# Optimization experiments

Measured on AMD Instinct MI355X. Metric: run time of the kernel, lower is better.

The kernel has to match this reference:

```python
import jax, jax.numpy as jnp
import numpy as np

S = 3      # num_subset
CI = 64    # inter_channels
C = 256    # in_channels == out_channels
T = 400    # num_frame
V = 25     # num_node


def make_pe(channel, joint_num, time_len, domain):
    if domain == 'temporal':
        pos = np.repeat(np.arange(time_len), joint_num).astype(np.float32)
    else:
        pos = np.tile(np.arange(joint_num), time_len).astype(np.float32)
    pe = np.zeros((time_len * joint_num, channel), dtype=np.float32)
    div = np.exp(np.arange(0, channel, 2, dtype=np.float32) * (-np.log(10000.0) / channel))
    pe[:, 0::2] = np.sin(pos[:, None] * div[None, :])
    pe[:, 1::2] = np.cos(pos[:, None] * div[None, :])
    pe = pe.reshape(time_len, joint_num, channel).transpose(2, 0, 1)[None]  # (1,C,T,V)
    return jnp.asarray(pe)


def setup_inputs() -> dict:
    key = jax.random.key(0)
    ks = jax.random.split(key, 10)
    def w(k, shape):
        return jax.random.normal(k, shape, jnp.float32) * 0.02
    return {
        'x': jax.random.normal(ks[0], (4, C, T, V), jnp.float32),
        'x1': jax.random.normal(ks[1], (4, C, T, V), jnp.float32),
        'pe_s': make_pe(C, V, T, 'spatial'),
        'pe_t': make_pe(C, V, T, 'temporal'),
        'in_nets_W': w(ks[2], (2 * S * CI, C)), 'in_nets_b': jnp.zeros((2 * S * CI,), jnp.float32),
        'alphas': jnp.ones((1, S, 1, 1), jnp.float32),
        'attention0s': jnp.ones((1, S, V, V), jnp.float32) / V,
        'out_nets_W': w(ks[3], (C, S * C)), 'out_nets_b': jnp.zeros((C,), jnp.float32),
        'out_nets_g': jnp.ones((C,), jnp.float32), 'out_nets_beta': jnp.zeros((C,), jnp.float32),
        'ff_nets_W': w(ks[4], (C, C)), 'ff_nets_b': jnp.zeros((C,), jnp.float32),
        'ff_nets_g': jnp.ones((C,), jnp.float32), 'ff_nets_beta': jnp.zeros((C,), jnp.float32),
        'in_nett_W': w(ks[5], (2 * S * CI, C)), 'in_nett_b': jnp.zeros((2 * S * CI,), jnp.float32),
        'alphat': jnp.ones((1, S, 1, 1), jnp.float32),
        'attention0t': jnp.broadcast_to(jnp.eye(T, dtype=jnp.float32), (1, S, T, T)),
        'out_nett_W': w(ks[6], (C, S * C)), 'out_nett_b': jnp.zeros((C,), jnp.float32),
        'out_nett_g': jnp.ones((C,), jnp.float32), 'out_nett_beta': jnp.zeros((C,), jnp.float32),
        'ff_nett_W': w(ks[7], (C, C)), 'ff_nett_b': jnp.zeros((C,), jnp.float32),
        'ff_nett_g': jnp.ones((C,), jnp.float32), 'ff_nett_beta': jnp.zeros((C,), jnp.float32),
        'case': 0,
    }


def _conv1x1(W, b, x):
    return jnp.einsum('oc,nctv->notv', W, x) + b[None, :, None, None]

def _bn(x, g, b):  # eval-mode BN (running mean 0, var 1) -> channel affine
    return x * g[None, :, None, None] + b[None, :, None, None]

def _lrelu(x):
    return jnp.where(x >= 0, x, 0.1 * x)


def reference(x, x1, pe_s, pe_t, in_nets_W, in_nets_b, alphas, attention0s,
              out_nets_W, out_nets_b, out_nets_g, out_nets_beta,
              ff_nets_W, ff_nets_b, ff_nets_g, ff_nets_beta,
              in_nett_W, in_nett_b, alphat, attention0t,
              out_nett_W, out_nett_b, out_nett_g, out_nett_beta,
              ff_nett_W, ff_nett_b, ff_nett_g, ff_nett_beta, case):
    # case == 0 path of the original forward (dropout p=0 -> identity).
    def spatial(xi):
        y = xi + pe_s  # spatial positional encoding
        def half(xh, yh):  # xh, yh: (2, C, T, V) half-batch, as in x.view(2,2,C,T,V)
            qk = _conv1x1(in_nets_W, in_nets_b, yh).reshape(2, 2 * S, CI, T, V)
            q, k = qk[:, :S], qk[:, S:]
            att = jnp.tanh(jnp.einsum('nsctu,nsctv->nsuv', q, k) / (CI * T)) * alphas + attention0s
            return jnp.einsum('nctv,nsvw->nsctw', xh, att).reshape(2, S * C, T, V)
        z = jnp.concatenate([half(xi[:2], y[:2]), half(xi[2:], y[2:])], axis=0)
        h = _lrelu(xi + _bn(_conv1x1(out_nets_W, out_nets_b, z), out_nets_g, out_nets_beta))
        return _lrelu(xi + _bn(_conv1x1(ff_nets_W, ff_nets_b, h), ff_nets_g, ff_nets_beta))

    def temporal(yi):
        z = yi + pe_t  # temporal positional encoding
        def half(yh, zh):
            qk = _conv1x1(in_nett_W, in_nett_b, zh).reshape(2, 2 * S, CI, T, V)
            q, k = qk[:, :S], qk[:, S:]
            att = jnp.tanh(jnp.einsum('nsctv,nscqv->nstq', q, k) / (CI * V)) * alphat + attention0t
            return jnp.einsum('nctv,nstq->nscqv', yh, att).reshape(2, S * C, T, V)
        z2 = jnp.concatenate([half(yi[:2], z[:2]), half(yi[2:], z[2:])], axis=0)
        h = _lrelu(yi + _bn(_conv1x1(out_nett_W, out_nett_b, z2), out_nett_g, out_nett_beta))
        return _lrelu(yi + _bn(_conv1x1(ff_nett_W, ff_nett_b, h), ff_nett_g, ff_nett_beta))

    out0 = temporal(spatial(x))
    out1 = temporal(spatial(x1))
    return jnp.stack([out0, out1], axis=0)  # (2, 4, C, T, V)
```

## Files before the change

### kernel.cpp

```cpp
#include <hip/hip_runtime.h>
#include <math.h>


#define PP 10000
#define SAMP 2560000

typedef __attribute__((ext_vector_type(8))) __bf16 bf16x8;
typedef __attribute__((ext_vector_type(4))) float f32x4;

#define LIDX(g, r) ((g) * 128 + ((r) ^ (g)))

__device__ __forceinline__ float4 ld4(const float* p) { return *(const float4*)p; }
__device__ __forceinline__ float lrelu(float v) { return v >= 0.f ? v : 0.1f * v; }

template<int MODE, bool PE, bool BGLOB, bool OUTGLOB>
__global__ __launch_bounds__(256)
void gemm_mfma(const float* __restrict__ W, int Kw,
               const float* __restrict__ bias,
               const float* __restrict__ g, const float* __restrict__ beta,
               const float* __restrict__ bg0, const float* __restrict__ bg1,
               const float* __restrict__ bw,
               const float* __restrict__ pe,
               const float* rg0, const float* rg1,
               float* out, int n0, int M, int K)
{
    const int ln = blockIdx.z;
    const int ns = n0 + ln;
    const int p0 = blockIdx.x * 128;
    const int m0 = blockIdx.y * 128;
    const int tid = threadIdx.x;

    const float* Bp;
    if (BGLOB)
        Bp = (ns < 4) ? bg0 + (size_t)ns * (size_t)K * PP
                      : bg1 + (size_t)(ns - 4) * (size_t)K * PP;
    else
        Bp = bw + (size_t)ln * (size_t)K * PP;

    __shared__ __align__(16) bf16x8 AhL[512];
    __shared__ __align__(16) bf16x8 AlL[512];
    __shared__ __align__(16) bf16x8 BhL[512];
    __shared__ __align__(16) bf16x8 BlL[512];

    const int am  = tid >> 1;
    const int akb = (tid & 1) * 16;
    const int ag0 = akb >> 3;
    const float* wrow = W + (size_t)(m0 + am) * Kw + akb;

    const int bp  = tid & 127;
    const int bkg = (tid >> 7) * 8;
    const int bg_ = bkg >> 3;
    const int gp  = p0 + bp;
    const bool pok = gp < PP;

    const int lane = tid & 63;
    const int wv = tid >> 6;
    const int wr = (wv >> 1) * 64, wc = (wv & 1) * 64;
    const int lr = lane & 15;
    const int lg = lane >> 4;

    f32x4 acc[4][4];
#pragma unroll
    for (int i = 0; i < 4; i++)
#pragma unroll
        for (int j = 0; j < 4; j++) acc[i][j] = (f32x4){0.f, 0.f, 0.f, 0.f};

    float4 wreg[4];
    float  breg[2][8];

    auto loadAB = [&](int kc) {
#pragma unroll
        for (int q = 0; q < 4; q++) wreg[q] = ld4(wrow + kc + q * 4);
#pragma unroll
        for (int e = 0; e < 2; e++) {
            const int kk = kc + bkg + e * 16;
#pragma unroll
            for (int i = 0; i < 8; i++) {
                float v = 0.f;
                if (pok) {
                    v = Bp[(size_t)(kk + i) * PP + gp];
                    if (PE) v += pe[(size_t)(kk + i) * PP + gp];
                }
                breg[e][i] = v;
            }
        }
    };

    loadAB(0);

    for (int k0 = 0; k0 < K; k0 += 32) {
        {
            bf16x8 h0, h1, l0, l1;
#pragma unroll
            for (int q = 0; q < 4; q++) {
                const float vs0 = wreg[q].x, vs1 = wreg[q].y, vs2 = wreg[q].z, vs3 = wreg[q].w;
                __bf16 hh; const int ib = q * 4;
#define CVTA(c, val) { hh = (__bf16)(val); __bf16 ll = (__bf16)((val) - (float)hh); \
    if (ib + c < 8) { h0[ib + c] = hh; l0[ib + c] = ll; } else { h1[ib + c - 8] = hh; l1[ib + c - 8] = ll; } }
                CVTA(0, vs0) CVTA(1, vs1) CVTA(2, vs2) CVTA(3, vs3)
#undef CVTA
            }
            AhL[LIDX(ag0, am)]     = h0;
            AhL[LIDX(ag0 + 1, am)] = h1;
            AlL[LIDX(ag0, am)]     = l0;
            AlL[LIDX(ag0 + 1, am)] = l1;
        }
#pragma unroll
        for (int e = 0; e < 2; e++) {
            bf16x8 hb, lb;
#pragma unroll
            for (int i = 0; i < 8; i++) {
                __bf16 hh = (__bf16)breg[e][i];
                hb[i] = hh;
                lb[i] = (__bf16)(breg[e][i] - (float)hh);
            }
            BhL[LIDX(bg_ + 2 * e, bp)] = hb;
            BlL[LIDX(bg_ + 2 * e, bp)] = lb;
        }
        __syncthreads();

        const int kn = k0 + 32;
        if (kn < K) loadAB(kn);

        bf16x8 fbh[4], fbl[4];
#pragma unroll
        for (int fj = 0; fj < 4; fj++) {
            fbh[fj] = BhL[LIDX(lg, wc + fj * 16 + lr)];
            fbl[fj] = BlL[LIDX(lg, wc + fj * 16 + lr)];
        }
#pragma unroll
        for (int fi = 0; fi < 4; fi++) {
            bf16x8 fah = AhL[LIDX(lg, wr + fi * 16 + lr)];
            bf16x8 fal = AlL[LIDX(lg, wr + fi * 16 + lr)];
#pragma unroll
            for (int fj = 0; fj < 4; fj++) {
                acc[fi][fj] = __builtin_amdgcn_mfma_f32_16x16x32_bf16(fah, fbh[fj], acc[fi][fj], 0, 0, 0);
                acc[fi][fj] = __builtin_amdgcn_mfma_f32_16x16x32_bf16(fah, fbl[fj], acc[fi][fj], 0, 0, 0);
                acc[fi][fj] = __builtin_amdgcn_mfma_f32_16x16x32_bf16(fal, fbh[fj], acc[fi][fj], 0, 0, 0);
            }
        }
        __syncthreads();
    }

    const int rb = (lane >> 4) * 4;

    if (MODE == 5) {
#pragma unroll
        for (int fi = 0; fi < 4; fi++) {
            const int mb = m0 + wr + fi * 16 + rb;
            const int sec = mb >> 6, cl = mb & 63;
            float* qt = out + (size_t)ln * 3840000ull + (size_t)sec * 640000ull + cl;
            const float b0 = bias[mb], b1 = bias[mb + 1], b2 = bias[mb + 2], b3 = bias[mb + 3];
#pragma unroll
            for (int fj = 0; fj < 4; fj++) {
                const int p = p0 + wc + fj * 16 + lr;
                if (p >= PP) continue;
                const int t = p / 25, v = p - t * 25;
                f32x4 a = acc[fi][fj];
                *(float4*)(qt + (size_t)t * 1600 + v * 64) =
                    make_float4(a[0] + b0, a[1] + b1, a[2] + b2, a[3] + b3);
            }
        }
        return;
    }

    float* op = out + (OUTGLOB ? (size_t)ns : (size_t)ln) * (size_t)M * PP;
    const float* resp = nullptr;
    if (MODE == 1 || MODE == 4)
        resp = (ns < 4) ? rg0 + (size_t)ns * SAMP : rg1 + (size_t)(ns - 4) * SAMP;

#pragma unroll
    for (int fi = 0; fi < 4; fi++) {
#pragma unroll
        for (int r = 0; r < 4; r++) {
            const int m = m0 + wr + fi * 16 + rb + r;
            const float bi = (MODE == 0 || MODE == 1 || MODE == 4) ? bias[m] : 0.f;
            const float gi = (MODE == 1 || MODE == 4) ? g[m] : 0.f;
            const float be = (MODE == 1 || MODE == 4) ? beta[m] : 0.f;
            const size_t rowoff = (size_t)m * PP;
#pragma unroll
            for (int fj = 0; fj < 4; fj++) {
                const int p = p0 + wc + fj * 16 + lr;
                if (p >= PP) continue;
                const float a = acc[fi][fj][r];
                float val;
                if (MODE == 0)      val = a + bi;
                else if (MODE == 2) val = a;
                else if (MODE == 3) val = op[rowoff + p] + a;
                else if (MODE == 4) val = lrelu(resp[rowoff + p] + gi * (op[rowoff + p] + a + bi) + be);
                else                val = lrelu(resp[rowoff + p] + gi * (a + bi) + be);
                op[rowoff + p] = val;
            }
        }
    }
}

__global__ __launch_bounds__(256)
void apply_t_mfma(const float* __restrict__ y, const float* __restrict__ attT,
                  float* __restrict__ z, int n0, int s)
{
    const int ln = blockIdx.z;
    const int ns = n0 + ln;
    const int j0 = blockIdx.x * 128;
    const int q0 = blockIdx.y * 128;
    const float* A = attT + ((size_t)ln * 3 + s) * 160000ull;
    const float* Y = y + (size_t)ns * SAMP;
    float* zout = z + (size_t)ln * SAMP;
    const int tid = threadIdx.x;

    __shared__ __align__(16) bf16x8 AhL[512];
    __shared__ __align__(16) bf16x8 AlL[512];
    __shared__ __align__(16) bf16x8 BhL[512];
    __shared__ __align__(16) bf16x8 BlL[512];

    const int am  = tid >> 1;
    const int akb = (tid & 1) * 16;
    const int ag0 = akb >> 3;
    const int qA  = q0 + am;
    const float* arow = A + (size_t)qA * 400;

    const int bp  = tid & 127;
    const int bkg = (tid >> 7) * 8;
    const int bg_ = bkg >> 3;
    const int j   = j0 + bp;
    const int cB  = j / 25, vB = j % 25;
    const float* yrow = Y + (size_t)cB * PP + vB;

    const int lane = tid & 63;
    const int wv = tid >> 6;
    const int wr = (wv >> 1) * 64, wc = (wv & 1) * 64;
    const int lr = lane & 15;
    const int lg = lane >> 4;

    f32x4 acc[4][4];
#pragma unroll
    for (int i = 0; i < 4; i++)
#pragma unroll
        for (int jj = 0; jj < 4; jj++) acc[i][jj] = (f32x4){0.f, 0.f, 0.f, 0.f};

    float4 wreg[4];
    float  breg[2][8];

    auto loadAB = [&](int kc) {
#pragma unroll
        for (int q = 0; q < 4; q++) {
            const int ks_ = kc + akb + q * 4;
            float4 v = make_float4(0.f, 0.f, 0.f, 0.f);
            if (qA < 400 && ks_ < 400) v = ld4(arow + ks_);
            wreg[q] = v;
        }
#pragma unroll
        for (int e = 0; e < 2; e++) {
            const int kb = kc + bkg + e * 16;
#pragma unroll
            for (int i = 0; i < 8; i++) {
                const int t = kb + i;
                breg[e][i] = (t < 400) ? yrow[(size_t)t * 25] : 0.f;
            }
        }
    };

    loadAB(0);

    for (int k0 = 0; k0 < 416; k0 += 32) {
        {
            bf16x8 h0, h1, l0, l1;
#pragma unroll
            for (int q = 0; q < 4; q++) {
                const float vs0 = wreg[q].x, vs1 = wreg[q].y, vs2 = wreg[q].z, vs3 = wreg[q].w;
                __bf16 hh; const int ib = q * 4;
#define CVTA(c, val) { hh = (__bf16)(val); __bf16 ll = (__bf16)((val) - (float)hh); \
    if (ib + c < 8) { h0[ib + c] = hh; l0[ib + c] = ll; } else { h1[ib + c - 8] = hh; l1[ib + c - 8] = ll; } }
                CVTA(0, vs0) CVTA(1, vs1) CVTA(2, vs2) CVTA(3, vs3)
#undef CVTA
            }
            AhL[LIDX(ag0, am)]     = h0;
            AhL[LIDX(ag0 + 1, am)] = h1;
            AlL[LIDX(ag0, am)]     = l0;
            AlL[LIDX(ag0 + 1, am)] = l1;
        }
#pragma unroll
        for (int e = 0; e < 2; e++) {
            bf16x8 hb, lb;
#pragma unroll
            for (int i = 0; i < 8; i++) {
                __bf16 hh = (__bf16)breg[e][i];
                hb[i] = hh;
                lb[i] = (__bf16)(breg[e][i] - (float)hh);
            }
            BhL[LIDX(bg_ + 2 * e, bp)] = hb;
            BlL[LIDX(bg_ + 2 * e, bp)] = lb;
        }
        __syncthreads();

        const int kn = k0 + 32;
        if (kn < 416) loadAB(kn);

        bf16x8 fbh[4], fbl[4];
#pragma unroll
        for (int fj = 0; fj < 4; fj++) {
            fbh[fj] = BhL[LIDX(lg, wc + fj * 16 + lr)];
            fbl[fj] = BlL[LIDX(lg, wc + fj * 16 + lr)];
        }
#pragma unroll
        for (int fi = 0; fi < 4; fi++) {
            bf16x8 fah = AhL[LIDX(lg, wr + fi * 16 + lr)];
            bf16x8 fal = AlL[LIDX(lg, wr + fi * 16 + lr)];
#pragma unroll
            for (int fj = 0; fj < 4; fj++) {
                acc[fi][fj] = __builtin_amdgcn_mfma_f32_16x16x32_bf16(fah, fbh[fj], acc[fi][fj], 0, 0, 0);
                acc[fi][fj] = __builtin_amdgcn_mfma_f32_16x16x32_bf16(fah, fbl[fj], acc[fi][fj], 0, 0, 0);
                acc[fi][fj] = __builtin_amdgcn_mfma_f32_16x16x32_bf16(fal, fbh[fj], acc[fi][fj], 0, 0, 0);
            }
        }
        __syncthreads();
    }

    const int rb = (lane >> 4) * 4;
#pragma unroll
    for (int fi = 0; fi < 4; fi++) {
#pragma unroll
        for (int r = 0; r < 4; r++) {
            const int q = q0 + wr + fi * 16 + rb + r;
            if (q >= 400) continue;
#pragma unroll
            for (int fj = 0; fj < 4; fj++) {
                const int p = j0 + wc + fj * 16 + lr;
                const int c = p / 25, v = p - c * 25;
                zout[(size_t)c * PP + (size_t)q * 25 + v] = acc[fi][fj][r];
            }
        }
    }
}

__global__ __launch_bounds__(256)
void scores_t_mfma(const float* __restrict__ qkT,
                   const float* __restrict__ alphat,
                   const float* __restrict__ att0t,
                   float* __restrict__ aT)
{
    const int idx = blockIdx.y;
    const int s = idx % 3, ln = idx / 3;
    const int t0 = (blockIdx.x & 3) * 128;
    const int q0 = (blockIdx.x >> 2) * 128;
    const float* base = qkT + (size_t)ln * 3840000ull;
    const float* Aq = base + (size_t)(3 + s) * 640000ull;
    const float* Bt = base + (size_t)s * 640000ull;
    const int tid = threadIdx.x;

    __shared__ __align__(16) bf16x8 AhL[512];
    __shared__ __align__(16) bf16x8 AlL[512];
    __shared__ __align__(16) bf16x8 BhL[512];
    __shared__ __align__(16) bf16x8 BlL[512];

    const int am  = tid >> 1;
    const int akb = (tid & 1) * 16;
    const int ag0 = akb >> 3;
    const int qA  = q0 + am;
    const int tB  = t0 + am;
    const float* arow = Aq + (size_t)qA * 1600 + akb;
    const float* brow = Bt + (size_t)tB * 1600 + akb;
    const bool aok = qA < 400;
    const bool bok = tB < 400;

    const int lane = tid & 63;
    const int wv = tid >> 6;
    const int wr = (wv >> 1) * 64, wc = (wv & 1) * 64;
    const int lr = lane & 15;
    const int lg = lane >> 4;

    f32x4 acc[4][4];
#pragma unroll
    for (int i = 0; i < 4; i++)
#pragma unroll
        for (int j = 0; j < 4; j++) acc[i][j] = (f32x4){0.f, 0.f, 0.f, 0.f};

    float4 areg[4], brg[4];
    auto loadAB = [&](int kc) {
#pragma unroll
        for (int q = 0; q < 4; q++) {
            areg[q] = aok ? ld4(arow + kc + q * 4) : make_float4(0.f, 0.f, 0.f, 0.f);
            brg[q]  = bok ? ld4(brow + kc + q * 4) : make_float4(0.f, 0.f, 0.f, 0.f);
        }
    };

    loadAB(0);

    for (int k0 = 0; k0 < 1600; k0 += 32) {
        {
            bf16x8 h0, h1, l0, l1;
#pragma unroll
            for (int q = 0; q < 4; q++) {
                const float vs0 = areg[q].x, vs1 = areg[q].y, vs2 = areg[q].z, vs3 = areg[q].w;
                __bf16 hh; const int ib = q * 4;
#define CVTA(c, val) { hh = (__bf16)(val); __bf16 ll = (__bf16)((val) - (float)hh); \
    if (ib + c < 8) { h0[ib + c] = hh; l0[ib + c] = ll; } else { h1[ib + c - 8] = hh; l1[ib + c - 8] = ll; } }
                CVTA(0, vs0) CVTA(1, vs1) CVTA(2, vs2) CVTA(3, vs3)
#undef CVTA
            }
            AhL[LIDX(ag0, am)]     = h0;
            AhL[LIDX(ag0 + 1, am)] = h1;
            AlL[LIDX(ag0, am)]     = l0;
            AlL[LIDX(ag0 + 1, am)] = l1;
        }
        {
            bf16x8 h0, h1, l0, l1;
#pragma unroll
            for (int q = 0; q < 4; q++) {
                const float vs0 = brg[q].x, vs1 = brg[q].y, vs2 = brg[q].z, vs3 = brg[q].w;
                __bf16 hh; const int ib = q * 4;
#define CVTB(c, val) { hh = (__bf16)(val); __bf16 ll = (__bf16)((val) - (float)hh); \
    if (ib + c < 8) { h0[ib + c] = hh; l0[ib + c] = ll; } else { h1[ib + c - 8] = hh; l1[ib + c - 8] = ll; } }
                CVTB(0, vs0) CVTB(1, vs1) CVTB(2, vs2) CVTB(3, vs3)
#undef CVTB
            }
            BhL[LIDX(ag0, am)]     = h0;
            BhL[LIDX(ag0 + 1, am)] = h1;
            BlL[LIDX(ag0, am)]     = l0;
            BlL[LIDX(ag0 + 1, am)] = l1;
        }
        __syncthreads();

        const int kn = k0 + 32;
        if (kn < 1600) loadAB(kn);

        bf16x8 fbh[4], fbl[4];
#pragma unroll
        for (int fj = 0; fj < 4; fj++) {
            fbh[fj] = BhL[LIDX(lg, wc + fj * 16 + lr)];
            fbl[fj] = BlL[LIDX(lg, wc + fj * 16 + lr)];
        }
#pragma unroll
        for (int fi = 0; fi < 4; fi++) {
            bf16x8 fah = AhL[LIDX(lg, wr + fi * 16 + lr)];
            bf16x8 fal = AlL[LIDX(lg, wr + fi * 16 + lr)];
#pragma unroll
            for (int fj = 0; fj < 4; fj++) {
                acc[fi][fj] = __builtin_amdgcn_mfma_f32_16x16x32_bf16(fah, fbh[fj], acc[fi][fj], 0, 0, 0);
                acc[fi][fj] = __builtin_amdgcn_mfma_f32_16x16x32_bf16(fah, fbl[fj], acc[fi][fj], 0, 0, 0);
                acc[fi][fj] = __builtin_amdgcn_mfma_f32_16x16x32_bf16(fal, fbh[fj], acc[fi][fj], 0, 0, 0);
            }
        }
        __syncthreads();
    }

    const int rb = (lane >> 4) * 4;
    const float al = alphat[s];
    float* aTp = aT + (size_t)idx * 160000ull;
    const float* a0p = att0t + (size_t)s * 160000ull;

#pragma unroll
    for (int fi = 0; fi < 4; fi++) {
        const int qb = q0 + wr + fi * 16 + rb;
#pragma unroll
        for (int fj = 0; fj < 4; fj++) {
            const int t = t0 + wc + fj * 16 + lr;
            if (t >= 400) continue;
#pragma unroll
            for (int r = 0; r < 4; r++) {
                const int q = qb + r;
                if (q >= 400) continue;
                aTp[(size_t)q * 400 + t] =
                    tanhf(acc[fi][fj][r] * (1.f / 1600.f)) * al + a0p[(size_t)t * 400 + q];
            }
        }
    }
}

__global__ __launch_bounds__(256)
void scores_s_partial(const float* __restrict__ qk, float* __restrict__ part)
{
    const int chunk = blockIdx.x, s = blockIdx.y, ln = blockIdx.z;
    const float* qsec = qk + ((size_t)ln * 384 + s * 64) * PP + (size_t)chunk * 3200;
    const float* ksec = qk + ((size_t)ln * 384 + (3 + s) * 64) * PP + (size_t)chunk * 3200;
    __shared__ float QL[3200];
    __shared__ float KL[3200];
    const int tid = threadIdx.x;
    for (int i = tid; i < 3200; i += 256) {
        QL[i] = qsec[i];
        KL[i] = ksec[i];
    }
    __syncthreads();
    const int o0 = tid, o1 = tid + 256, o2 = tid + 512;
    const int u0 = o0 / 25, v0 = o0 % 25;
    const int u1 = o1 / 25, v1 = o1 % 25;
    const int u2 = o2 / 25, v2 = o2 % 25;
    float a0 = 0.f, a1 = 0.f, a2 = 0.f;
#pragma unroll 8
    for (int r = 0; r < 128; r++) {
        int ro = r * 25;
        a0 = fmaf(QL[ro + u0], KL[ro + v0], a0);
        a1 = fmaf(QL[ro + u1], KL[ro + v1], a1);
        if (tid < 113) a2 = fmaf(QL[ro + u2], KL[ro + v2], a2);
    }
    float* pp = part + (((size_t)(ln * 3 + s)) * 200 + chunk) * 625;
    pp[o0] = a0;
    pp[o1] = a1;
    if (tid < 113) pp[o2] = a2;
}

__global__ void scores_s_final(const float* __restrict__ part,
                               const float* __restrict__ alphas,
                               const float* __restrict__ att0s,
                               float* __restrict__ atts)
{
    const int idx = blockIdx.x;
    const int s = idx % 3;
    const int o = threadIdx.x;
    if (o >= 625) return;
    const float* pb = part + (size_t)idx * 200 * 625 + o;
    float sum = 0.f;
#pragma unroll 8
    for (int i = 0; i < 200; i++) sum += pb[(size_t)i * 625];
    atts[(size_t)idx * 625 + o] = tanhf(sum * (1.f / 25600.f)) * alphas[s] + att0s[s * 625 + o];
}

__global__ __launch_bounds__(256)
void apply_s_kernel(const float* __restrict__ x0, const float* __restrict__ x1,
                    const float* __restrict__ atts, float* __restrict__ z,
                    int n0, int s)
{
    const int ln = blockIdx.y;
    const int ns = n0 + ln;
    const int tid = threadIdx.x;
    __shared__ float attL[700];
    for (int i = tid; i < 700; i += 256) attL[i] = 0.f;
    __syncthreads();
    for (int i = tid; i < 625; i += 256) {
        int v = i / 25, w = i % 25;
        attL[v * 28 + w] = atts[(size_t)ln * 1875 + s * 625 + i];
    }
    __syncthreads();
    const float* xp = (ns < 4) ? x0 + (size_t)ns * SAMP : x1 + (size_t)(ns - 4) * SAMP;
    const int r0 = (blockIdx.x * 256 + tid) * 2;
    const float* xr0 = xp + (size_t)r0 * 25;
    float xr[2][25];
#pragma unroll
    for (int i = 0; i < 2; i++)
#pragma unroll
        for (int v = 0; v < 25; v++) xr[i][v] = xr0[i * 25 + v];
    const int c0 = r0 / 400, t0 = r0 % 400;

    float4 acc0[7], acc1[7];
#pragma unroll
    for (int w4 = 0; w4 < 7; w4++) {
        acc0[w4] = make_float4(0.f, 0.f, 0.f, 0.f);
        acc1[w4] = make_float4(0.f, 0.f, 0.f, 0.f);
    }
#pragma unroll
    for (int v = 0; v < 25; v++) {
        const float4* arow = (const float4*)&attL[v * 28];
        float xv0 = xr[0][v], xv1 = xr[1][v];
#pragma unroll
        for (int w4 = 0; w4 < 7; w4++) {
            float4 a = arow[w4];
            acc0[w4].x = fmaf(xv0, a.x, acc0[w4].x);
            acc0[w4].y = fmaf(xv0, a.y, acc0[w4].y);
            acc0[w4].z = fmaf(xv0, a.z, acc0[w4].z);
            acc0[w4].w = fmaf(xv0, a.w, acc0[w4].w);
            acc1[w4].x = fmaf(xv1, a.x, acc1[w4].x);
            acc1[w4].y = fmaf(xv1, a.y, acc1[w4].y);
            acc1[w4].z = fmaf(xv1, a.z, acc1[w4].z);
            acc1[w4].w = fmaf(xv1, a.w, acc1[w4].w);
        }
    }
    float* zp = z + (size_t)ln * SAMP + (size_t)c0 * PP + (size_t)t0 * 25;
#pragma unroll
    for (int w4 = 0; w4 < 7; w4++) {
        int wb = w4 * 4;
        if (wb + 0 < 25) zp[wb + 0] = acc0[w4].x;
        if (wb + 1 < 25) zp[wb + 1] = acc0[w4].y;
        if (wb + 2 < 25) zp[wb + 2] = acc0[w4].z;
        if (wb + 3 < 25) zp[wb + 3] = acc0[w4].w;
    }
#pragma unroll
    for (int w4 = 0; w4 < 7; w4++) {
        int wb = w4 * 4;
        if (wb + 0 < 25) zp[25 + wb + 0] = acc1[w4].x;
        if (wb + 1 < 25) zp[25 + wb + 1] = acc1[w4].y;
        if (wb + 2 < 25) zp[25 + wb + 2] = acc1[w4].z;
        if (wb + 3 < 25) zp[25 + wb + 3] = acc1[w4].w;
    }
}

extern "C" void kernel_launch(void* const* d_in, const int* in_sizes, int n_in,
                              void* d_out, int out_size, void* d_ws, size_t ws_size,
                              hipStream_t stream)
{
    const float* x    = (const float*)d_in[0];
    const float* x1   = (const float*)d_in[1];
    const float* pe_s = (const float*)d_in[2];
    const float* pe_t = (const float*)d_in[3];
    const float* Wsi  = (const float*)d_in[4];
    const float* bsi  = (const float*)d_in[5];
    const float* alphas = (const float*)d_in[6];
    const float* att0s  = (const float*)d_in[7];
    const float* Wso  = (const float*)d_in[8];
    const float* bso  = (const float*)d_in[9];
    const float* gso  = (const float*)d_in[10];
    const float* beso = (const float*)d_in[11];
    const float* Wsf  = (const float*)d_in[12];
    const float* bsf  = (const float*)d_in[13];
    const float* gsf  = (const float*)d_in[14];
    const float* besf = (const float*)d_in[15];
    const float* Wti  = (const float*)d_in[16];
    const float* bti  = (const float*)d_in[17];
    const float* alphat = (const float*)d_in[18];
    const float* att0t  = (const float*)d_in[19];
    const float* Wto  = (const float*)d_in[20];
    const float* bto  = (const float*)d_in[21];
    const float* gto  = (const float*)d_in[22];
    const float* beto = (const float*)d_in[23];
    const float* Wtf  = (const float*)d_in[24];
    const float* btf  = (const float*)d_in[25];
    const float* gtf  = (const float*)d_in[26];
    const float* betf = (const float*)d_in[27];

    float* outp = (float*)d_out;
    const float* outpB = outp + 4ull * SAMP;

    int G = 1;
    for (int g = 8; g >= 1; g >>= 1) {
        if ((size_t)g * 27587500ull <= ws_size) { G = g; break; }
    }

    float* A   = (float*)d_ws;
    float* Zs  = A  + (size_t)G * 3840000ull;
    float* aT  = Zs + (size_t)G * 2560000ull;
    float* sp  = aT + (size_t)G * 480000ull;
    float* as  = sp + (size_t)G * 15000ull;

    dim3 blk(256);
    for (int n0 = 0; n0 < 8; n0 += G) {
        dim3 gIn(79, 3, G), gOut(79, 2, G);

        gemm_mfma<0, true, true, false><<<gIn, blk, 0, stream>>>(
            Wsi, 256, bsi, nullptr, nullptr, x, x1, nullptr, pe_s,
            nullptr, nullptr, A, n0, 384, 256);
        scores_s_partial<<<dim3(200, 3, G), blk, 0, stream>>>(A, Zs);
        scores_s_final<<<dim3(3 * G), dim3(640), 0, stream>>>(Zs, alphas, att0s, as);
        for (int s = 0; s < 3; s++) {
            apply_s_kernel<<<dim3(200, G), blk, 0, stream>>>(x, x1, as, Zs, n0, s);
            if (s == 0)
                gemm_mfma<2, false, false, false><<<gOut, blk, 0, stream>>>(
                    Wso + s * 256, 768, nullptr, nullptr, nullptr, nullptr, nullptr, Zs,
                    nullptr, nullptr, nullptr, A, n0, 256, 256);
            else if (s == 1)
                gemm_mfma<3, false, false, false><<<gOut, blk, 0, stream>>>(
                    Wso + s * 256, 768, nullptr, nullptr, nullptr, nullptr, nullptr, Zs,
                    nullptr, nullptr, nullptr, A, n0, 256, 256);
            else
                gemm_mfma<4, false, false, false><<<gOut, blk, 0, stream>>>(
                    Wso + s * 256, 768, bso, gso, beso, nullptr, nullptr, Zs,
                    nullptr, x, x1, A, n0, 256, 256);
        }
        gemm_mfma<1, false, false, true><<<gOut, blk, 0, stream>>>(
            Wsf, 256, bsf, gsf, besf, nullptr, nullptr, A, nullptr,
            x, x1, outp, n0, 256, 256);

        gemm_mfma<5, true, true, false><<<gIn, blk, 0, stream>>>(
            Wti, 256, bti, nullptr, nullptr, outp, outpB, nullptr, pe_t,
            nullptr, nullptr, A, n0, 384, 256);
        scores_t_mfma<<<dim3(16, 3 * G), blk, 0, stream>>>(A, alphat, att0t, aT);
        for (int s = 0; s < 3; s++) {
            apply_t_mfma<<<dim3(50, 4, G), blk, 0, stream>>>(outp, aT, Zs, n0, s);
            if (s == 0)
                gemm_mfma<2, false, false, false><<<gOut, blk, 0, stream>>>(
                    Wto + s * 256, 768, nullptr, nullptr, nullptr, nullptr, nullptr, Zs,
                    nullptr, nullptr, nullptr, A, n0, 256, 256);
            else if (s == 1)
                gemm_mfma<3, false, false, false><<<gOut, blk, 0, stream>>>(
                    Wto + s * 256, 768, nullptr, nullptr, nullptr, nullptr, nullptr, Zs,
                    nullptr, nullptr, nullptr, A, n0, 256, 256);
            else
                gemm_mfma<4, false, false, false><<<gOut, blk, 0, stream>>>(
                    Wto + s * 256, 768, bto, gto, beto, nullptr, nullptr, Zs,
                    nullptr, outp, outpB, A, n0, 256, 256);
        }
        gemm_mfma<1, false, false, true><<<gOut, blk, 0, stream>>>(
            Wtf, 256, btf, gtf, betf, nullptr, nullptr, A, nullptr,
            outp, outpB, outp, n0, 256, 256);
    }
}
```

Before: 2.124 ms.

## Double-buffer LDS tiles in MFMA GEMMs and swap grid axes for reuse

The three MFMA GEMM kernels (gemm_mfma, apply_t_mfma, scores_t_mfma) get two LDS buffers and two register stages. This lets the next K-slice load and bf16 split overlap with the MFMA on the current slice, and removes one barrier per K step. The grid is also transposed so the M (or q) tile index moves fastest. Blocks that share the same B/activation columns then run together, which should improve L2 reuse. The cost is doubled LDS use and more registers, which may lower occupancy. The K loop bounds now assume K is a multiple of 64 (apply_t pads to 448).

```diff
diff --git a/kernel.cpp b/kernel.cpp
--- a/kernel.cpp
+++ b/kernel.cpp
@@ -26,8 +26,8 @@
 {
     const int ln = blockIdx.z;
     const int ns = n0 + ln;
-    const int p0 = blockIdx.x * 128;
-    const int m0 = blockIdx.y * 128;
+    const int m0 = blockIdx.x * 128;
+    const int p0 = blockIdx.y * 128;
     const int tid = threadIdx.x;
 
     const float* Bp;
@@ -37,10 +37,10 @@
     else
         Bp = bw + (size_t)ln * (size_t)K * PP;
 
-    __shared__ __align__(16) bf16x8 AhL[512];
-    __shared__ __align__(16) bf16x8 AlL[512];
-    __shared__ __align__(16) bf16x8 BhL[512];
-    __shared__ __align__(16) bf16x8 BlL[512];
+    __shared__ __align__(16) bf16x8 AhL[2][512];
+    __shared__ __align__(16) bf16x8 AlL[2][512];
+    __shared__ __align__(16) bf16x8 BhL[2][512];
+    __shared__ __align__(16) bf16x8 BlL[2][512];
 
     const int am  = tid >> 1;
     const int akb = (tid & 1) * 16;
@@ -65,12 +65,14 @@
 #pragma unroll
         for (int j = 0; j < 4; j++) acc[i][j] = (f32x4){0.f, 0.f, 0.f, 0.f};
 
-    float4 wreg[4];
-    float  breg[2][8];
-
-    auto loadAB = [&](int kc) {
+    float4 wregA[4], wregB[4];
+    float  bregA[2][8], bregB[2][8];
+
+    auto loadW = [&](int kc, float4* wreg) {
 #pragma unroll
         for (int q = 0; q < 4; q++) wreg[q] = ld4(wrow + kc + q * 4);
+    };
+    auto loadBv = [&](int kc, float breg[2][8]) {
 #pragma unroll
         for (int e = 0; e < 2; e++) {
             const int kk = kc + bkg + e * 16;
@@ -85,26 +87,23 @@
             }
         }
     };
-
-    loadAB(0);
-
-    for (int k0 = 0; k0 < K; k0 += 32) {
-        {
-            bf16x8 h0, h1, l0, l1;
-#pragma unroll
-            for (int q = 0; q < 4; q++) {
-                const float vs0 = wreg[q].x, vs1 = wreg[q].y, vs2 = wreg[q].z, vs3 = wreg[q].w;
-                __bf16 hh; const int ib = q * 4;
+    auto stageA = [&](const float4* wreg, int buf) {
+        bf16x8 h0, h1, l0, l1;
+#pragma unroll
+        for (int q = 0; q < 4; q++) {
+            const float vs0 = wreg[q].x, vs1 = wreg[q].y, vs2 = wreg[q].z, vs3 = wreg[q].w;
+            __bf16 hh; const int ib = q * 4;
 #define CVTA(c, val) { hh = (__bf16)(val); __bf16 ll = (__bf16)((val) - (float)hh); \
     if (ib + c < 8) { h0[ib + c] = hh; l0[ib + c] = ll; } else { h1[ib + c - 8] = hh; l1[ib + c - 8] = ll; } }
-                CVTA(0, vs0) CVTA(1, vs1) CVTA(2, vs2) CVTA(3, vs3)
+            CVTA(0, vs0) CVTA(1, vs1) CVTA(2, vs2) CVTA(3, vs3)
 #undef CVTA
-            }
-            AhL[LIDX(ag0, am)]     = h0;
-            AhL[LIDX(ag0 + 1, am)] = h1;
-            AlL[LIDX(ag0, am)]     = l0;
-            AlL[LIDX(ag0 + 1, am)] = l1;
-        }
+        }
+        AhL[buf][LIDX(ag0, am)]     = h0;
+        AhL[buf][LIDX(ag0 + 1, am)] = h1;
+        AlL[buf][LIDX(ag0, am)]     = l0;
+        AlL[buf][LIDX(ag0 + 1, am)] = l1;
+    };
+    auto stageB = [&](const float breg[2][8], int buf) {
 #pragma unroll
         for (int e = 0; e < 2; e++) {
             bf16x8 hb, lb;
@@ -114,24 +113,21 @@
                 hb[i] = hh;
                 lb[i] = (__bf16)(breg[e][i] - (float)hh);
             }
-            BhL[LIDX(bg_ + 2 * e, bp)] = hb;
-            BlL[LIDX(bg_ + 2 * e, bp)] = lb;
-        }
-        __syncthreads();
-
-        const int kn = k0 + 32;
-        if (kn < K) loadAB(kn);
-
+            BhL[buf][LIDX(bg_ + 2 * e, bp)] = hb;
+            BlL[buf][LIDX(bg_ + 2 * e, bp)] = lb;
+        }
+    };
+    auto domfma = [&](int buf) {
         bf16x8 fbh[4], fbl[4];
 #pragma unroll
         for (int fj = 0; fj < 4; fj++) {
-            fbh[fj] = BhL[LIDX(lg, wc + fj * 16 + lr)];
-            fbl[fj] = BlL[LIDX(lg, wc + fj * 16 + lr)];
+            fbh[fj] = BhL[buf][LIDX(lg, wc + fj * 16 + lr)];
+            fbl[fj] = BlL[buf][LIDX(lg, wc + fj * 16 + lr)];
         }
 #pragma unroll
         for (int fi = 0; fi < 4; fi++) {
-            bf16x8 fah = AhL[LIDX(lg, wr + fi * 16 + lr)];
-            bf16x8 fal = AlL[LIDX(lg, wr + fi * 16 + lr)];
+            bf16x8 fah = AhL[buf][LIDX(lg, wr + fi * 16 + lr)];
+            bf16x8 fal = AlL[buf][LIDX(lg, wr + fi * 16 + lr)];
 #pragma unroll
             for (int fj = 0; fj < 4; fj++) {
                 acc[fi][fj] = __builtin_amdgcn_mfma_f32_16x16x32_bf16(fah, fbh[fj], acc[fi][fj], 0, 0, 0);
@@ -139,7 +135,21 @@
                 acc[fi][fj] = __builtin_amdgcn_mfma_f32_16x16x32_bf16(fal, fbh[fj], acc[fi][fj], 0, 0, 0);
             }
         }
+    };
+
+    loadW(0, wregA); loadBv(0, bregA);
+    int buf = 0;
+    for (int k0 = 0; k0 < K; k0 += 64) {
+        if (k0 + 32 < K) { loadW(k0 + 32, wregB); loadBv(k0 + 32, bregB); }
+        stageA(wregA, buf); stageB(bregA, buf);
         __syncthreads();
+        domfma(buf);
+        buf ^= 1;
+        if (k0 + 64 < K) { loadW(k0 + 64, wregA); loadBv(k0 + 64, bregA); }
+        stageA(wregB, buf); stageB(bregB, buf);
+        __syncthreads();
+        domfma(buf);
+        buf ^= 1;
     }
 
     const int rb = (lane >> 4) * 4;
@@ -201,17 +211,17 @@
 {
     const int ln = blockIdx.z;
     const int ns = n0 + ln;
-    const int j0 = blockIdx.x * 128;
-    const int q0 = blockIdx.y * 128;
+    const int q0 = blockIdx.x * 128;
+    const int j0 = blockIdx.y * 128;
     const float* A = attT + ((size_t)ln * 3 + s) * 160000ull;
     const float* Y = y + (size_t)ns * SAMP;
     float* zout = z + (size_t)ln * SAMP;
     const int tid = threadIdx.x;
 
-    __shared__ __align__(16) bf16x8 AhL[512];
-    __shared__ __align__(16) bf16x8 AlL[512];
-    __shared__ __align__(16) bf16x8 BhL[512];
-    __shared__ __align__(16) bf16x8 BlL[512];
+    __shared__ __align__(16) bf16x8 AhL[2][512];
+    __shared__ __align__(16) bf16x8 AlL[2][512];
+    __shared__ __align__(16) bf16x8 BhL[2][512];
+    __shared__ __align__(16) bf16x8 BlL[2][512];
 
     const int am  = tid >> 1;
     const int akb = (tid & 1) * 16;
@@ -238,10 +248,10 @@
 #pragma unroll
         for (int jj = 0; jj < 4; jj++) acc[i][jj] = (f32x4){0.f, 0.f, 0.f, 0.f};
 
-    float4 wreg[4];
-    float  breg[2][8];
-
-    auto loadAB = [&](int kc) {
+    float4 wregA[4], wregB[4];
+    float  bregA[2][8], bregB[2][8];
+
+    auto loadW = [&](int kc, float4* wreg) {
 #pragma unroll
         for (int q = 0; q < 4; q++) {
             const int ks_ = kc + akb + q * 4;
@@ -249,6 +259,8 @@
             if (qA < 400 && ks_ < 400) v = ld4(arow + ks_);
             wreg[q] = v;
         }
+    };
+    auto loadBv = [&](int kc, float breg[2][8]) {
 #pragma unroll
         for (int e = 0; e < 2; e++) {
             const int kb = kc + bkg + e * 16;
@@ -259,26 +271,23 @@
             }
         }
     };
-
-    loadAB(0);
-
-    for (int k0 = 0; k0 < 416; k0 += 32) {
-        {
-            bf16x8 h0, h1, l0, l1;
-#pragma unroll
-            for (int q = 0; q < 4; q++) {
-                const float vs0 = wreg[q].x, vs1 = wreg[q].y, vs2 = wreg[q].z, vs3 = wreg[q].w;
-                __bf16 hh; const int ib = q * 4;
+    auto stageA = [&](const float4* wreg, int buf) {
+        bf16x8 h0, h1, l0, l1;
+#pragma unroll
+        for (int q = 0; q < 4; q++) {
+            const float vs0 = wreg[q].x, vs1 = wreg[q].y, vs2 = wreg[q].z, vs3 = wreg[q].w;
+            __bf16 hh; const int ib = q * 4;
 #define CVTA(c, val) { hh = (__bf16)(val); __bf16 ll = (__bf16)((val) - (float)hh); \
     if (ib + c < 8) { h0[ib + c] = hh; l0[ib + c] = ll; } else { h1[ib + c - 8] = hh; l1[ib + c - 8] = ll; } }
-                CVTA(0, vs0) CVTA(1, vs1) CVTA(2, vs2) CVTA(3, vs3)
+            CVTA(0, vs0) CVTA(1, vs1) CVTA(2, vs2) CVTA(3, vs3)
 #undef CVTA
-            }
-            AhL[LIDX(ag0, am)]     = h0;
-            AhL[LIDX(ag0 + 1, am)] = h1;
-            AlL[LIDX(ag0, am)]     = l0;
-            AlL[LIDX(ag0 + 1, am)] = l1;
-        }
+        }
+        AhL[buf][LIDX(ag0, am)]     = h0;
+        AhL[buf][LIDX(ag0 + 1, am)] = h1;
+        AlL[buf][LIDX(ag0, am)]     = l0;
+        AlL[buf][LIDX(ag0 + 1, am)] = l1;
+    };
+    auto stageB = [&](const float breg[2][8], int buf) {
 #pragma unroll
         for (int e = 0; e < 2; e++) {
             bf16x8 hb, lb;
@@ -288,24 +297,21 @@
                 hb[i] = hh;
                 lb[i] = (__bf16)(breg[e][i] - (float)hh);
             }
-            BhL[LIDX(bg_ + 2 * e, bp)] = hb;
-            BlL[LIDX(bg_ + 2 * e, bp)] = lb;
-        }
-        __syncthreads();
-
-        const int kn = k0 + 32;
-        if (kn < 416) loadAB(kn);
-
+            BhL[buf][LIDX(bg_ + 2 * e, bp)] = hb;
+            BlL[buf][LIDX(bg_ + 2 * e, bp)] = lb;
+        }
+    };
+    auto domfma = [&](int buf) {
         bf16x8 fbh[4], fbl[4];
 #pragma unroll
         for (int fj = 0; fj < 4; fj++) {
-            fbh[fj] = BhL[LIDX(lg, wc + fj * 16 + lr)];
-            fbl[fj] = BlL[LIDX(lg, wc + fj * 16 + lr)];
+            fbh[fj] = BhL[buf][LIDX(lg, wc + fj * 16 + lr)];
+            fbl[fj] = BlL[buf][LIDX(lg, wc + fj * 16 + lr)];
         }
 #pragma unroll
         for (int fi = 0; fi < 4; fi++) {
-            bf16x8 fah = AhL[LIDX(lg, wr + fi * 16 + lr)];
-            bf16x8 fal = AlL[LIDX(lg, wr + fi * 16 + lr)];
+            bf16x8 fah = AhL[buf][LIDX(lg, wr + fi * 16 + lr)];
+            bf16x8 fal = AlL[buf][LIDX(lg, wr + fi * 16 + lr)];
 #pragma unroll
             for (int fj = 0; fj < 4; fj++) {
                 acc[fi][fj] = __builtin_amdgcn_mfma_f32_16x16x32_bf16(fah, fbh[fj], acc[fi][fj], 0, 0, 0);
@@ -313,7 +319,21 @@
                 acc[fi][fj] = __builtin_amdgcn_mfma_f32_16x16x32_bf16(fal, fbh[fj], acc[fi][fj], 0, 0, 0);
             }
         }
+    };
+
+    loadW(0, wregA); loadBv(0, bregA);
+    int buf = 0;
+    for (int k0 = 0; k0 < 448; k0 += 64) {
+        if (k0 + 32 < 448) { loadW(k0 + 32, wregB); loadBv(k0 + 32, bregB); }
+        stageA(wregA, buf); stageB(bregA, buf);
         __syncthreads();
+        domfma(buf);
+        buf ^= 1;
+        if (k0 + 64 < 448) { loadW(k0 + 64, wregA); loadBv(k0 + 64, bregA); }
+        stageA(wregB, buf); stageB(bregB, buf);
+        __syncthreads();
+        domfma(buf);
+        buf ^= 1;
     }
 
     const int rb = (lane >> 4) * 4;
@@ -348,10 +368,10 @@
     const float* Bt = base + (size_t)s * 640000ull;
     const int tid = threadIdx.x;
 
-    __shared__ __align__(16) bf16x8 AhL[512];
-    __shared__ __align__(16) bf16x8 AlL[512];
-    __shared__ __align__(16) bf16x8 BhL[512];
-    __shared__ __align__(16) bf16x8 BlL[512];
+    __shared__ __align__(16) bf16x8 AhL[2][512];
+    __shared__ __align__(16) bf16x8 AlL[2][512];
+    __shared__ __align__(16) bf16x8 BhL[2][512];
+    __shared__ __align__(16) bf16x8 BlL[2][512];
 
     const int am  = tid >> 1;
     const int akb = (tid & 1) * 16;
@@ -375,18 +395,16 @@
 #pragma unroll
         for (int j = 0; j < 4; j++) acc[i][j] = (f32x4){0.f, 0.f, 0.f, 0.f};
 
-    float4 areg[4], brg[4];
-    auto loadAB = [&](int kc) {
+    float4 aregA[4], brgA[4], aregB[4], brgB[4];
+
+    auto loadAB = [&](int kc, float4* areg, float4* brg) {
 #pragma unroll
         for (int q = 0; q < 4; q++) {
             areg[q] = aok ? ld4(arow + kc + q * 4) : make_float4(0.f, 0.f, 0.f, 0.f);
             brg[q]  = bok ? ld4(brow + kc + q * 4) : make_float4(0.f, 0.f, 0.f, 0.f);
         }
     };
-
-    loadAB(0);
-
-    for (int k0 = 0; k0 < 1600; k0 += 32) {
+    auto stageAB = [&](const float4* areg, const float4* brg, int buf) {
         {
             bf16x8 h0, h1, l0, l1;
 #pragma unroll
@@ -398,10 +416,10 @@
                 CVTA(0, vs0) CVTA(1, vs1) CVTA(2, vs2) CVTA(3, vs3)
 #undef CVTA
             }
-            AhL[LIDX(ag0, am)]     = h0;
-            AhL[LIDX(ag0 + 1, am)] = h1;
-            AlL[LIDX(ag0, am)]     = l0;
-            AlL[LIDX(ag0 + 1, am)] = l1;
+            AhL[buf][LIDX(ag0, am)]     = h0;
+            AhL[buf][LIDX(ag0 + 1, am)] = h1;
+            AlL[buf][LIDX(ag0, am)]     = l0;
+            AlL[buf][LIDX(ag0 + 1, am)] = l1;
         }
         {
             bf16x8 h0, h1, l0, l1;
@@ -414,26 +432,23 @@
                 CVTB(0, vs0) CVTB(1, vs1) CVTB(2, vs2) CVTB(3, vs3)
 #undef CVTB
             }
-            BhL[LIDX(ag0, am)]     = h0;
-            BhL[LIDX(ag0 + 1, am)] = h1;
-            BlL[LIDX(ag0, am)]     = l0;
-            BlL[LIDX(ag0 + 1, am)] = l1;
-        }
-        __syncthreads();
-
-        const int kn = k0 + 32;
-        if (kn < 1600) loadAB(kn);
-
+            BhL[buf][LIDX(ag0, am)]     = h0;
+            BhL[buf][LIDX(ag0 + 1, am)] = h1;
+            BlL[buf][LIDX(ag0, am)]     = l0;
+            BlL[buf][LIDX(ag0 + 1, am)] = l1;
+        }
+    };
+    auto domfma = [&](int buf) {
         bf16x8 fbh[4], fbl[4];
 #pragma unroll
         for (int fj = 0; fj < 4; fj++) {
-            fbh[fj] = BhL[LIDX(lg, wc + fj * 16 + lr)];
-            fbl[fj] = BlL[LIDX(lg, wc + fj * 16 + lr)];
+            fbh[fj] = BhL[buf][LIDX(lg, wc + fj * 16 + lr)];
+            fbl[fj] = BlL[buf][LIDX(lg, wc + fj * 16 + lr)];
         }
 #pragma unroll
         for (int fi = 0; fi < 4; fi++) {
-            bf16x8 fah = AhL[LIDX(lg, wr + fi * 16 + lr)];
-            bf16x8 fal = AlL[LIDX(lg, wr + fi * 16 + lr)];
+            bf16x8 fah = AhL[buf][LIDX(lg, wr + fi * 16 + lr)];
+            bf16x8 fal = AlL[buf][LIDX(lg, wr + fi * 16 + lr)];
 #pragma unroll
             for (int fj = 0; fj < 4; fj++) {
                 acc[fi][fj] = __builtin_amdgcn_mfma_f32_16x16x32_bf16(fah, fbh[fj], acc[fi][fj], 0, 0, 0);
@@ -441,7 +456,21 @@
                 acc[fi][fj] = __builtin_amdgcn_mfma_f32_16x16x32_bf16(fal, fbh[fj], acc[fi][fj], 0, 0, 0);
             }
         }
+    };
+
+    loadAB(0, aregA, brgA);
+    int buf = 0;
+    for (int k0 = 0; k0 < 1600; k0 += 64) {
+        if (k0 + 32 < 1600) loadAB(k0 + 32, aregB, brgB);
+        stageAB(aregA, brgA, buf);
         __syncthreads();
+        domfma(buf);
+        buf ^= 1;
+        if (k0 + 64 < 1600) loadAB(k0 + 64, aregA, brgA);
+        stageAB(aregB, brgB, buf);
+        __syncthreads();
+        domfma(buf);
+        buf ^= 1;
     }
 
     const int rb = (lane >> 4) * 4;
@@ -632,7 +661,7 @@
 
     dim3 blk(256);
     for (int n0 = 0; n0 < 8; n0 += G) {
-        dim3 gIn(79, 3, G), gOut(79, 2, G);
+        dim3 gIn(3, 79, G), gOut(2, 79, G);
 
         gemm_mfma<0, true, true, false><<<gIn, blk, 0, stream>>>(
             Wsi, 256, bsi, nullptr, nullptr, x, x1, nullptr, pe_s,
@@ -663,7 +692,7 @@
             nullptr, nullptr, A, n0, 384, 256);
         scores_t_mfma<<<dim3(16, 3 * G), blk, 0, stream>>>(A, alphat, att0t, aT);
         for (int s = 0; s < 3; s++) {
-            apply_t_mfma<<<dim3(50, 4, G), blk, 0, stream>>>(outp, aT, Zs, n0, s);
+            apply_t_mfma<<<dim3(4, 50, G), blk, 0, stream>>>(outp, aT, Zs, n0, s);
             if (s == 0)
                 gemm_mfma<2, false, false, false><<<gOut, blk, 0, stream>>>(
                     Wto + s * 256, 768, nullptr, nullptr, nullptr, nullptr, nullptr, Zs,
```

Measured after the change: 3.076 ms. 1.45x slower.
